# Performance work log

Measured on AMD Instinct MI355X. Metric: run time of the kernel, lower is better.

Reference implementation:

```python
import jax, jax.numpy as jnp
import numpy as np

# fbank band edges (hp.bandmode == 'fbank'), 32 bands over 257 freq bins
EBAND = [0,3,5,8,10,13,15,18,22,25,29,33,38,42,48,53,59,66,73,80,89,97,107,117,128,140,153,167,183,199,216,256]

def _inverse_filter():
    f = np.zeros((len(EBAND), EBAND[-1] + 1), np.float32)
    for i in range(len(EBAND) - 1):
        w = EBAND[i + 1] - EBAND[i]
        for j in range(w):
            f[i, EBAND[i] + j] = 1.0 - j / w
            f[i + 1, EBAND[i] + j] = j / w
    return jnp.asarray(f)  # [32, 257]

def _glin(x, w):
    # GroupedLinear (DeepFilterNet-style, no bias): w [g, in/g, out/g]
    g, gi, go = w.shape
    y = jnp.einsum('...gi,gio->...go', x.reshape(x.shape[:-1] + (g, gi)), w)
    return y.reshape(x.shape[:-1] + (g * go,))

def _prelu(x, a):
    return jnp.where(x >= 0, x, a * x)

def _gru(x, wih, whh, bih, bhh):
    # single-layer torch-style GRU; x [T,B,I], wih/whh [3H, I/H]
    H = whh.shape[-1]
    h0 = jnp.zeros((x.shape[1], H), x.dtype)
    def step(h, xt):
        gi = xt @ wih.T + bih
        gh = h @ whh.T + bhh
        ir, iz, inn = jnp.split(gi, 3, axis=-1)
        hr, hz, hn = jnp.split(gh, 3, axis=-1)
        r = jax.nn.sigmoid(ir + hr)
        z = jax.nn.sigmoid(iz + hz)
        n = jnp.tanh(inn + r * hn)
        hnew = (1.0 - z) * n + z * h
        return hnew, hnew
    _, ys = jax.lax.scan(step, h0, x)
    return ys  # [T,B,H]

def _ggru_layer(x, wih, whh, bih, bhh):
    # grouped GRU layer: weights stacked on leading group axis
    g = wih.shape[0]
    T, B, I = x.shape
    xg = x.reshape(T, B, g, I // g).transpose(2, 0, 1, 3)  # [g,T,B,I/g]
    ys = jax.vmap(_gru)(xg, wih, whh, bih, bhh)            # [g,T,B,H/g]
    return ys.transpose(1, 2, 0, 3).reshape(T, B, -1)

def _shuffle(x, g):
    # channel shuffle between grouped GRU layers
    T, B, H = x.shape
    return x.reshape(T, B, -1, g).swapaxes(2, 3).reshape(T, B, H)

def _forward(main_input, spec, log_power_input, s1_fc_in_w, s1_fc_in_b,
             s1_gru_wih0, s1_gru_whh0, s1_gru_bih0, s1_gru_bhh0,
             s1_gru_wih1, s1_gru_whh1, s1_gru_bih1, s1_gru_bhh1,
             s1_fcout_w, fc_in_low_w, prelu_low, fc_in_high_w, prelu_high,
             gru_low_wih, gru_low_whh, gru_low_bih, gru_low_bhh,
             gru_high_wih, gru_high_whh, gru_high_bih, gru_high_bhh,
             fc_out_low_w, fc_out_high_w, ne, fc):
    B, _, T, F = main_input.shape
    # --- Stage1: pad time, unfold window, keep first ne+1 taps ---
    xp = jnp.pad(main_input, ((0, 0), (0, 0), (ne, ne), (0, 0)))
    win = jnp.stack([xp[:, :, k:k + T] for k in range(ne + 1)], axis=-1)  # [B,1,T,F,ne+1]
    x = win.reshape(B, T, F * (ne + 1))                                   # [B,T,64]
    x0 = (x @ s1_fc_in_w.T + s1_fc_in_b).transpose(1, 0, 2)               # [T,B,32]
    y1 = _gru(x0, s1_gru_wih0, s1_gru_whh0, s1_gru_bih0, s1_gru_bhh0)
    y2 = _gru(y1, s1_gru_wih1, s1_gru_whh1, s1_gru_bih1, s1_gru_bhh1)
    x1 = (y1 + y2).transpose(1, 0, 2)                                     # add_outputs; [B,T,32]
    band_mask = jax.nn.sigmoid(_glin(x1, s1_fcout_w))                     # [B,T,32]
    full_mask = (band_mask @ _inverse_filter()).transpose(0, 2, 1)        # [B,257,T]
    out = spec * full_mask[..., None]                                     # [B,257,T,2]
    # --- low band path ---
    low = jnp.concatenate([log_power_input[:, :, :fc], band_mask], axis=-1)  # [B,T,160]
    low = _prelu(_glin(low, fc_in_low_w), prelu_low).transpose(1, 0, 2)      # [T,B,64]
    acc = jnp.zeros_like(low)
    inp = low
    for l in range(2):  # 2 grouped layers, shuffle between, add_outputs
        inp = _ggru_layer(inp, gru_low_wih[l], gru_low_whh[l], gru_low_bih[l], gru_low_bhh[l])
        if l == 0:
            inp = _shuffle(inp, 2)
        acc = acc + inp
    mask_low = jax.nn.sigmoid(_glin(acc.transpose(1, 0, 2), fc_out_low_w))   # [B,T,128]
    # --- high band path ---
    high = jnp.concatenate([log_power_input[:, :, fc:256], band_mask], axis=-1)  # [B,T,160]
    high = _prelu(_glin(high, fc_in_high_w), prelu_high).transpose(1, 0, 2)      # [T,B,32]
    dfh = _ggru_layer(high, gru_high_wih, gru_high_whh, gru_high_bih, gru_high_bhh)
    mask_high = jax.nn.sigmoid(_glin(dfh.transpose(1, 0, 2), fc_out_high_w))     # [B,T,128]
    # --- fuse masks (rows: 0:fc low, fc:256 high, 256 passthrough) ---
    mask = jnp.concatenate([
        mask_low.transpose(0, 2, 1) * full_mask[:, :fc],
        mask_high.transpose(0, 2, 1) * full_mask[:, fc:256],
        full_mask[:, 256:257],
    ], axis=1)                                                            # [B,257,T]
    spec_out = mask[..., None] * out
    spec_mag = jnp.sqrt(spec_out[..., 0] ** 2 + spec_out[..., 1] ** 2)
    return full_mask, mask, spec_mag, spec_out

def setup_inputs():
    ks = iter(jax.random.split(jax.random.key(0), 48))
    rn = lambda shape, s=1.0: jax.random.normal(next(ks), shape, jnp.float32) * s
    B, T = 256, 256
    return {
        'main_input': rn((B, 1, T, 32)),
        'spec': rn((B, 257, T, 2)),
        'log_power_input': rn((B, T, 256)),
        'n_expand_fbank': 1,
        'freq_cut': 128,
        's1_fc_in_w': rn((32, 64), 0.125),
        's1_fc_in_b': rn((32,), 0.05),
        's1_gru_wih0': rn((96, 32), 0.18),
        's1_gru_whh0': rn((96, 32), 0.18),
        's1_gru_bih0': rn((96,), 0.05),
        's1_gru_bhh0': rn((96,), 0.05),
        's1_gru_wih1': rn((96, 32), 0.18),
        's1_gru_whh1': rn((96, 32), 0.18),
        's1_gru_bih1': rn((96,), 0.05),
        's1_gru_bhh1': rn((96,), 0.05),
        's1_fcout_w': rn((1, 32, 32), 0.18),
        'fc_in_low_w': rn((1, 160, 64), 0.08),
        'prelu_low': jnp.full((1,), 0.25, jnp.float32),
        'fc_in_high_w': rn((2, 80, 16), 0.11),
        'prelu_high': jnp.full((1,), 0.25, jnp.float32),
        'gru_low_wih': rn((2, 2, 96, 32), 0.18),
        'gru_low_whh': rn((2, 2, 96, 32), 0.18),
        'gru_low_bih': rn((2, 2, 96), 0.05),
        'gru_low_bhh': rn((2, 2, 96), 0.05),
        'gru_high_wih': rn((2, 48, 16), 0.25),
        'gru_high_whh': rn((2, 48, 16), 0.25),
        'gru_high_bih': rn((2, 48), 0.05),
        'gru_high_bhh': rn((2, 48), 0.05),
        'fc_out_low_w': rn((1, 64, 128), 0.125),
        'fc_out_high_w': rn((2, 16, 64), 0.25),
    }

def reference(main_input, spec, log_power_input, n_expand_fbank, freq_cut,
              s1_fc_in_w, s1_fc_in_b,
              s1_gru_wih0, s1_gru_whh0, s1_gru_bih0, s1_gru_bhh0,
              s1_gru_wih1, s1_gru_whh1, s1_gru_bih1, s1_gru_bhh1,
              s1_fcout_w, fc_in_low_w, prelu_low, fc_in_high_w, prelu_high,
              gru_low_wih, gru_low_whh, gru_low_bih, gru_low_bhh,
              gru_high_wih, gru_high_whh, gru_high_bih, gru_high_bhh,
              fc_out_low_w, fc_out_high_w):
    return _forward(main_input, spec, log_power_input, s1_fc_in_w, s1_fc_in_b,
                    s1_gru_wih0, s1_gru_whh0, s1_gru_bih0, s1_gru_bhh0,
                    s1_gru_wih1, s1_gru_whh1, s1_gru_bih1, s1_gru_bhh1,
                    s1_fcout_w, fc_in_low_w, prelu_low, fc_in_high_w, prelu_high,
                    gru_low_wih, gru_low_whh, gru_low_bih, gru_low_bhh,
                    gru_high_wih, gru_high_whh, gru_high_bih, gru_high_bhh,
                    fc_out_low_w, fc_out_high_w, int(n_expand_fbank), int(freq_cut))
```

## Files before the change

kernel.cpp:

```cpp
#include <hip/hip_runtime.h>
#include <math.h>

#define Bn 256
#define Tn 256

__constant__ int EB[32] = {0,3,5,8,10,13,15,18,22,25,29,33,38,42,48,53,59,66,73,80,89,97,107,117,128,140,153,167,183,199,216,256};

__device__ __forceinline__ float fsig(float x){ return __builtin_amdgcn_rcpf(1.f + __expf(-x)); }
__device__ __forceinline__ float ftanh(float x){ return 1.f - 2.f*__builtin_amdgcn_rcpf(1.f + __expf(2.f*x)); }

__device__ __forceinline__ void gload16(const float* g, float* l){
  __builtin_amdgcn_global_load_lds((const __attribute__((address_space(1))) void*)g,
                                   (__attribute__((address_space(3))) void*)l, 16, 0, 0);
}

#define KEEP(x) asm volatile("" : "+v"(x))

#define DOT16(res, X, W) do{ float _s0=0.f,_s1=0.f,_s2=0.f,_s3=0.f; \
  _Pragma("unroll") for (int _e=0;_e<4;++_e){ \
    _s0=fmaf((X)[_e],(W)[_e],_s0); _s1=fmaf((X)[4+_e],(W)[4+_e],_s1); \
    _s2=fmaf((X)[8+_e],(W)[8+_e],_s2); _s3=fmaf((X)[12+_e],(W)[12+_e],_s3);} \
  (res)=(_s0+_s1)+(_s2+_s3); }while(0)

#define DOT8(res, X, W) do{ float _s0=0.f,_s1=0.f; \
  _Pragma("unroll") for (int _e=0;_e<4;++_e){ \
    _s0=fmaf((X)[_e],(W)[_e],_s0); _s1=fmaf((X)[4+_e],(W)[4+_e],_s1);} \
  (res)=_s0+_s1; }while(0)

#define FMA44(A, X, W) do{ \
  (A)[0]=fmaf((X).x,(W)[0].x,(A)[0]); (A)[1]=fmaf((X).x,(W)[0].y,(A)[1]); (A)[2]=fmaf((X).x,(W)[0].z,(A)[2]); (A)[3]=fmaf((X).x,(W)[0].w,(A)[3]); \
  (A)[0]=fmaf((X).y,(W)[1].x,(A)[0]); (A)[1]=fmaf((X).y,(W)[1].y,(A)[1]); (A)[2]=fmaf((X).y,(W)[1].z,(A)[2]); (A)[3]=fmaf((X).y,(W)[1].w,(A)[3]); \
  (A)[0]=fmaf((X).z,(W)[2].x,(A)[0]); (A)[1]=fmaf((X).z,(W)[2].y,(A)[1]); (A)[2]=fmaf((X).z,(W)[2].z,(A)[2]); (A)[3]=fmaf((X).z,(W)[2].w,(A)[3]); \
  (A)[0]=fmaf((X).w,(W)[3].x,(A)[0]); (A)[1]=fmaf((X).w,(W)[3].y,(A)[1]); (A)[2]=fmaf((X).w,(W)[3].z,(A)[2]); (A)[3]=fmaf((X).w,(W)[3].w,(A)[3]); \
}while(0)

#define FMA4V(P, AV, S) do{ (P).x=fmaf((AV).x,(S),(P).x); (P).y=fmaf((AV).y,(S),(P).y); \
  (P).z=fmaf((AV).z,(S),(P).z); (P).w=fmaf((AV).w,(S),(P).w); }while(0)

__global__ __launch_bounds__(256) void k0(const float* __restrict__ wfc, const float* __restrict__ bfc,
    const float* __restrict__ wih0, const float* __restrict__ bih0,
    const float* __restrict__ glw_ih, const float* __restrict__ glb_ih,
    const float* __restrict__ ghw_ih, const float* __restrict__ ghb_ih,
    float* __restrict__ wcT, float* __restrict__ bc,
    float* __restrict__ wBT, float* __restrict__ bB){
  int i = blockIdx.x*256 + threadIdx.x;
  if (i < 6144){
    int k = i/96, o = i - (i/96)*96;
    float s = 0.f;
    #pragma unroll
    for (int kk = 0; kk < 32; ++kk) s = fmaf(wih0[o*32+kk], wfc[kk*64+k], s);
    wcT[i] = s;
  } else if (i < 6240){
    int o = i - 6144;
    float s = bih0[o];
    #pragma unroll
    for (int kk = 0; kk < 32; ++kk) s = fmaf(wih0[o*32+kk], bfc[kk], s);
    bc[o] = s;
  } else if (i < 13920){
    int j = i - 6240;
    if (j < 6144){
      int og = j >> 7, rem = j & 127, k = rem >> 2, jj = rem & 3;
      int o = og*4 + jj; int g = o/96, r = o - g*96;
      wBT[j] = glw_ih[(g*96 + r)*32 + k];
    } else {
      int j2 = j - 6144;
      int oh = j2 >> 6, rem = j2 & 63, k = rem >> 2, jj = rem & 3;
      int o = oh*4 + jj; int g = o/48, r = o - g*48;
      wBT[j] = ghw_ih[(g*48 + r)*16 + k];
    }
  } else if (i < 14208){
    int o = i - 13920;
    bB[o] = (o < 192) ? glb_ih[o] : ghb_ih[o - 192];
  }
}

__global__ __launch_bounds__(256) void k1(const float* __restrict__ mi,
    const float* __restrict__ wcT, const float* __restrict__ bc,
    float* __restrict__ gi0){
  __shared__ float mbuf[33*36];
  const int tid = threadIdx.x;
  const int b = blockIdx.x >> 3;
  const int t0 = (blockIdx.x & 7)*32;
  const int bt0 = b*256 + t0;
  for (int idx = tid; idx < 264; idx += 256){
    int row = idx >> 3, c4 = idx & 7;
    int r = t0 - 1 + row;
    float4 v = make_float4(0.f,0.f,0.f,0.f);
    if (r >= 0) v = *(const float4*)&mi[(b*256 + r)*32 + c4*4];
    *(float4*)&mbuf[row*36 + c4*4] = v;
  }
  __syncthreads();
  const int og = tid >> 3, btg = tid & 7;
  if (og >= 24) return;
  float acc[4][4];
  #pragma unroll
  for (int bj = 0; bj < 4; ++bj){ acc[bj][0]=0.f; acc[bj][1]=0.f; acc[bj][2]=0.f; acc[bj][3]=0.f; }
  for (int fq = 0; fq < 8; ++fq){
    float4 wvp[4], wvc[4];
    #pragma unroll
    for (int i = 0; i < 4; ++i){
      int f = fq*4 + i;
      wvp[i] = *(const float4*)&wcT[(2*f)*96 + og*4];
      wvc[i] = *(const float4*)&wcT[(2*f+1)*96 + og*4];
    }
    #pragma unroll
    for (int bj = 0; bj < 4; ++bj){
      int btl = btg + 8*bj;
      float4 xp = *(const float4*)&mbuf[btl*36 + fq*4];
      float4 xc = *(const float4*)&mbuf[(btl+1)*36 + fq*4];
      FMA44(acc[bj], xp, wvp);
      FMA44(acc[bj], xc, wvc);
    }
  }
  float4 bias = *(const float4*)&bc[og*4];
  #pragma unroll
  for (int bj = 0; bj < 4; ++bj){
    int btl = btg + 8*bj;
    float4 o;
    o.x = acc[bj][0] + bias.x; o.y = acc[bj][1] + bias.y;
    o.z = acc[bj][2] + bias.z; o.w = acc[bj][3] + bias.w;
    *(float4*)&gi0[(bt0 + btl)*96 + og*4] = o;
  }
}

__global__ __launch_bounds__(128,1) void kSP(const float* __restrict__ gi0,
    const float* __restrict__ whh0, const float* __restrict__ bhh0,
    const float* __restrict__ wih1, const float* __restrict__ whh1,
    const float* __restrict__ bih1, const float* __restrict__ bhh1,
    const float* __restrict__ fco, float* __restrict__ bmA,
    const float* __restrict__ lpi,
    const float* __restrict__ wlo, const float* __restrict__ whi,
    float* __restrict__ pmid)
{
  __shared__ __attribute__((aligned(16))) float smem[8320];
  const int tid = threadIdx.x;
  if (blockIdx.x < 256){
    float* gib   = smem;
    float* y1buf = smem + 6144;
    float* h1arr = smem + 6208;
    float* h2arr = smem + 6240;
    const int wid = tid >> 6;
    const int lane = tid & 63;
    const int q = lane >> 5, h = lane & 31, ko = q*16;
    const int b = blockIdx.x;
    const float* gsrc = gi0 + b*24576;

    float wI[3][16], wH[3][16], wF[16];
    float b0, b1, b2, b3;
    if (wid == 0){
      #pragma unroll
      for (int g = 0; g < 3; ++g){
        const float* w = whh0 + (g*32+h)*32 + ko;
        #pragma unroll
        for (int k = 0; k < 16; ++k){ wI[g][k] = w[k]; wH[g][k] = w[k]; }
      }
      #pragma unroll
      for (int k = 0; k < 16; ++k) wF[k] = 0.f;
      b0 = bhh0[h]; b1 = bhh0[32+h]; b2 = bhh0[64+h]; b3 = 0.f;
      #pragma unroll
      for (int c0 = 0; c0 < 2; ++c0)
        for (int it = 0; it < 12; ++it)
          gload16(gsrc + c0*3072 + it*256 + lane*4, &gib[c0*3072 + it*256]);
      asm volatile("s_waitcnt vmcnt(0)" ::: "memory");
    } else {
      #pragma unroll
      for (int g = 0; g < 3; ++g){
        const float* wi = wih1 + (g*32+h)*32 + ko;
        const float* wh = whh1 + (g*32+h)*32 + ko;
        #pragma unroll
        for (int k = 0; k < 16; ++k){ wI[g][k] = wi[k]; wH[g][k] = wh[k]; }
      }
      #pragma unroll
      for (int k = 0; k < 16; ++k) wF[k] = fco[(ko+k)*32 + h];
      b0 = bih1[h] + bhh1[h];
      b1 = bih1[32+h] + bhh1[32+h];
      b2 = bih1[64+h];
      b3 = bhh1[64+h];
    }
    #pragma unroll
    for (int g = 0; g < 3; ++g){
      #pragma unroll
      for (int k = 0; k < 16; ++k){ KEEP(wI[g][k]); KEEP(wH[g][k]); }
    }
    #pragma unroll
    for (int k = 0; k < 16; ++k) KEEP(wF[k]);
    __syncthreads();

    float hv[16];
    #pragma unroll
    for (int k = 0; k < 16; ++k) hv[k] = 0.f;
    float hOwn = 0.f;
    float c_r = 0.f, c_z = 0.f, c_n = 0.f, p_r = 0.f, p_z = 0.f, p_n = 0.f;

    for (int s = 0; s <= Tn; ++s){
      __syncthreads();
      if (wid == 0){
        if (s < Tn){
          const int t = s;
          if ((t & 31) == 0){
            if (t){
              int c = t >> 5;
              if (c < 7){
                for (int it = 0; it < 12; ++it)
                  gload16(gsrc + (c+1)*3072 + it*256 + lane*4, &gib[((c+1)&1)*3072 + it*256]);
              }
            }
            const float* gt = &gib[((t>>5)&1)*3072 + (t&31)*96];
            c_r = gt[h]; c_z = gt[32+h]; c_n = gt[64+h];
          } else { c_r = p_r; c_z = p_z; c_n = p_n; }
          if ((t+1) & 31){
            const float* gn = &gib[(((t+1)>>5)&1)*3072 + ((t+1)&31)*96];
            p_r = gn[h]; p_z = gn[32+h]; p_n = gn[64+h];
          }
          float pr, pz, pn;
          DOT16(pr, hv, wI[0]); DOT16(pz, hv, wI[1]); DOT16(pn, hv, wI[2]);
          pr += __shfl_xor(pr,32); pz += __shfl_xor(pz,32); pn += __shfl_xor(pn,32);
          float r = fsig(c_r + pr + b0);
          float z = fsig(c_z + pz + b1);
          float nn = ftanh(c_n + r*(pn + b2));
          float hn = nn + z*(hOwn - nn);
          hOwn = hn;
          h1arr[h] = hn;
          if (q == 0) y1buf[(s & 1)*32 + h] = hn;
          *(float4*)&hv[0]  = *(const float4*)&h1arr[ko+0];
          *(float4*)&hv[4]  = *(const float4*)&h1arr[ko+4];
          *(float4*)&hv[8]  = *(const float4*)&h1arr[ko+8];
          *(float4*)&hv[12] = *(const float4*)&h1arr[ko+12];
        }
      } else {
        if (s >= 1){
          const int t = s - 1;
          const float* yb = &y1buf[(t & 1)*32];
          float xv[16];
          *(float4*)&xv[0]  = *(const float4*)&yb[ko+0];
          *(float4*)&xv[4]  = *(const float4*)&yb[ko+4];
          *(float4*)&xv[8]  = *(const float4*)&yb[ko+8];
          *(float4*)&xv[12] = *(const float4*)&yb[ko+12];
          float ur, uz, ui, vr, vz, vh;
          DOT16(ur, xv, wI[0]); DOT16(uz, xv, wI[1]); DOT16(ui, xv, wI[2]);
          DOT16(vr, hv, wH[0]); DOT16(vz, hv, wH[1]); DOT16(vh, hv, wH[2]);
          float qr = ur + vr, qz = uz + vz;
          qr += __shfl_xor(qr,32); qz += __shfl_xor(qz,32);
          ui += __shfl_xor(ui,32); vh += __shfl_xor(vh,32);
          float r1 = fsig(qr + b0);
          float z1 = fsig(qz + b1);
          float n1 = ftanh(ui + b2 + r1*(vh + b3));
          float hn = n1 + z1*(hOwn - n1);
          hOwn = hn;
          h2arr[h] = hn;
          *(float4*)&hv[0]  = *(const float4*)&h2arr[ko+0];
          *(float4*)&hv[4]  = *(const float4*)&h2arr[ko+4];
          *(float4*)&hv[8]  = *(const float4*)&h2arr[ko+8];
          *(float4*)&hv[12] = *(const float4*)&h2arr[ko+12];
          float sf = 0.f;
          #pragma unroll
          for (int k = 0; k < 16; ++k) sf = fmaf(xv[k] + hv[k], wF[k], sf);
          sf += __shfl_xor(sf,32);
          if (q == 0) bmA[(b*Tn + t)*32 + h] = fsig(sf);
        }
      }
    }
  } else {
    float* xb = smem;
    const int blk = blockIdx.x - 256;
    const int b = blk >> 3;
    const int t0 = (blk & 7)*32;
    const int bt0 = b*256 + t0;
    #pragma unroll
    for (int j = 0; j < 16; ++j){
      int idx = j*128 + tid;
      int row = idx >> 6, c4 = idx & 63;
      float4 v = *(const float4*)&lpi[(bt0 + row)*256 + c4*4];
      *(float4*)&xb[row*260 + c4*4] = v;
    }
    __syncthreads();
    const int og = tid >> 3, btg = tid & 7;
    for (int og2 = og; og2 < 24; og2 += 16){
      float acc[4][4];
      #pragma unroll
      for (int bj = 0; bj < 4; ++bj){ acc[bj][0]=0.f; acc[bj][1]=0.f; acc[bj][2]=0.f; acc[bj][3]=0.f; }
      int obase;
      if (og2 < 16){
        for (int kq = 0; kq < 32; ++kq){
          int k0_ = kq*4;
          float4 wv[4];
          #pragma unroll
          for (int i = 0; i < 4; ++i) wv[i] = *(const float4*)&wlo[(k0_+i)*64 + og2*4];
          #pragma unroll
          for (int bj = 0; bj < 4; ++bj){
            float4 xv = *(const float4*)&xb[(btg + 8*bj)*260 + k0_];
            FMA44(acc[bj], xv, wv);
          }
        }
        obase = og2*4;
      } else {
        int o0 = (og2 - 16)*4;
        int g = o0 >> 4, r0 = o0 & 15;
        int xoff = 128 + g*80;
        int nk = (g == 0) ? 20 : 12;
        for (int kq = 0; kq < nk; ++kq){
          int k0_ = kq*4;
          float4 wv[4];
          #pragma unroll
          for (int i = 0; i < 4; ++i) wv[i] = *(const float4*)&whi[(g*80 + k0_ + i)*16 + r0];
          #pragma unroll
          for (int bj = 0; bj < 4; ++bj){
            float4 xv = *(const float4*)&xb[(btg + 8*bj)*260 + xoff + k0_];
            FMA44(acc[bj], xv, wv);
          }
        }
        obase = 64 + o0;
      }
      #pragma unroll
      for (int bj = 0; bj < 4; ++bj){
        int btl = btg + 8*bj;
        float4 o;
        o.x = acc[bj][0]; o.y = acc[bj][1]; o.z = acc[bj][2]; o.w = acc[bj][3];
        *(float4*)&pmid[(bt0 + btl)*96 + obase] = o;
      }
    }
  }
}

__global__ __launch_bounds__(256) void kPb(const float* __restrict__ bmA,
    const float* __restrict__ pmid,
    const float* __restrict__ wlo, const float* __restrict__ plo,
    const float* __restrict__ whi, const float* __restrict__ phi,
    const float* __restrict__ wBT, const float* __restrict__ bB,
    float* __restrict__ giL, float* __restrict__ giH)
{
  __shared__ float bmb[32*36];
  __shared__ float mb[32*100];
  const int tid = threadIdx.x;
  const int b = blockIdx.x >> 3;
  const int t0 = (blockIdx.x & 7)*32;
  const int bt0 = b*256 + t0;
  {
    int row = tid >> 3, c4 = tid & 7;
    float4 v = *(const float4*)&bmA[(bt0 + row)*32 + c4*4];
    *(float4*)&bmb[row*36 + c4*4] = v;
  }
  __syncthreads();
  const int og = tid >> 3, btg = tid & 7;
  if (og < 16){
    float acc[4][4];
    #pragma unroll
    for (int bj = 0; bj < 4; ++bj){
      float4 p = *(const float4*)&pmid[(bt0 + btg + 8*bj)*96 + og*4];
      acc[bj][0] = p.x; acc[bj][1] = p.y; acc[bj][2] = p.z; acc[bj][3] = p.w;
    }
    for (int kq = 0; kq < 8; ++kq){
      int k0_ = kq*4;
      float4 wv[4];
      #pragma unroll
      for (int i = 0; i < 4; ++i) wv[i] = *(const float4*)&wlo[(128 + k0_ + i)*64 + og*4];
      #pragma unroll
      for (int bj = 0; bj < 4; ++bj){
        float4 xv = *(const float4*)&bmb[(btg + 8*bj)*36 + k0_];
        FMA44(acc[bj], xv, wv);
      }
    }
    const float a = plo[0];
    #pragma unroll
    for (int bj = 0; bj < 4; ++bj){
      float4 m;
      m.x = acc[bj][0] >= 0.f ? acc[bj][0] : a*acc[bj][0];
      m.y = acc[bj][1] >= 0.f ? acc[bj][1] : a*acc[bj][1];
      m.z = acc[bj][2] >= 0.f ? acc[bj][2] : a*acc[bj][2];
      m.w = acc[bj][3] >= 0.f ? acc[bj][3] : a*acc[bj][3];
      *(float4*)&mb[(btg + 8*bj)*100 + og*4] = m;
    }
  } else if (og < 24){
    int o0 = (og - 16)*4;
    int g = o0 >> 4, r0 = o0 & 15;
    float acc[4][4];
    #pragma unroll
    for (int bj = 0; bj < 4; ++bj){
      float4 p = *(const float4*)&pmid[(bt0 + btg + 8*bj)*96 + 64 + o0];
      acc[bj][0] = p.x; acc[bj][1] = p.y; acc[bj][2] = p.z; acc[bj][3] = p.w;
    }
    if (g == 1){
      for (int kq = 0; kq < 8; ++kq){
        int k0_ = 48 + kq*4;
        float4 wv[4];
        #pragma unroll
        for (int i = 0; i < 4; ++i) wv[i] = *(const float4*)&whi[(80 + k0_ + i)*16 + r0];
        #pragma unroll
        for (int bj = 0; bj < 4; ++bj){
          float4 xv = *(const float4*)&bmb[(btg + 8*bj)*36 + kq*4];
          FMA44(acc[bj], xv, wv);
        }
      }
    }
    const float a = phi[0];
    #pragma unroll
    for (int bj = 0; bj < 4; ++bj){
      float4 m;
      m.x = acc[bj][0] >= 0.f ? acc[bj][0] : a*acc[bj][0];
      m.y = acc[bj][1] >= 0.f ? acc[bj][1] : a*acc[bj][1];
      m.z = acc[bj][2] >= 0.f ? acc[bj][2] : a*acc[bj][2];
      m.w = acc[bj][3] >= 0.f ? acc[bj][3] : a*acc[bj][3];
      *(float4*)&mb[(btg + 8*bj)*100 + 64 + o0] = m;
    }
  }
  __syncthreads();
  for (int og2 = og; og2 < 72; og2 += 32){
    int woff, kbase, K, obase, dstride;
    float* dst;
    float4 bias;
    if (og2 < 48){
      woff = og2*128; kbase = (og2 >= 24) ? 32 : 0; K = 32;
      obase = og2*4; dst = giL; dstride = 192;
      bias = *(const float4*)&bB[obase];
    } else {
      int oh = og2 - 48;
      woff = 6144 + oh*64;
      int o0 = oh*4; int g = o0/48;
      kbase = 64 + g*16; K = 16;
      obase = o0; dst = giH; dstride = 96;
      bias = *(const float4*)&bB[192 + o0];
    }
    float acc[4][4];
    #pragma unroll
    for (int bj = 0; bj < 4; ++bj){ acc[bj][0]=0.f; acc[bj][1]=0.f; acc[bj][2]=0.f; acc[bj][3]=0.f; }
    for (int kq = 0; kq < K/4; ++kq){
      float4 wv[4];
      #pragma unroll
      for (int i = 0; i < 4; ++i) wv[i] = *(const float4*)&wBT[woff + (kq*4 + i)*4];
      #pragma unroll
      for (int bj = 0; bj < 4; ++bj){
        float4 xv = *(const float4*)&mb[(btg + 8*bj)*100 + kbase + kq*4];
        FMA44(acc[bj], xv, wv);
      }
    }
    #pragma unroll
    for (int bj = 0; bj < 4; ++bj){
      int btl = btg + 8*bj;
      float4 o;
      o.x = acc[bj][0] + bias.x; o.y = acc[bj][1] + bias.y;
      o.z = acc[bj][2] + bias.z; o.w = acc[bj][3] + bias.w;
      *(float4*)&dst[(bt0 + btl)*dstride + obase] = o;
    }
  }
}

__global__ __launch_bounds__(256,1) void kR2(const float* __restrict__ giL,
    const float* __restrict__ giH,
    const float* __restrict__ wihL, const float* __restrict__ whhL,
    const float* __restrict__ bihL, const float* __restrict__ bhhL,
    const float* __restrict__ whhH, const float* __restrict__ bhhH,
    float* __restrict__ acc, float* __restrict__ dfh)
{
  __shared__ __attribute__((aligned(16))) float smem[12544];
  const int tid = threadIdx.x;
  const int wid = tid >> 6;
  const int lane = tid & 63;
  if (blockIdx.x < 256){
    const int role = wid >> 1;
    const int g = wid & 1;
    const int q = lane >> 5, h = lane & 31, ko = q*16;
    const int b = blockIdx.x;
    float* gib   = smem + g*6144;
    float* y0buf = smem + 12288;
    float* h0arr = smem + 12416 + g*32;
    float* h1l   = smem + 12480;
    const float* gsrc = giL + b*49152 + g*96;

    float wI[3][16], wH[3][16];
    float b0, b1, b2, b3;
    if (role == 0){
      #pragma unroll
      for (int gt = 0; gt < 3; ++gt){
        const float* w = whhL + (g*96 + gt*32 + h)*32 + ko;
        #pragma unroll
        for (int k = 0; k < 16; ++k){ wI[gt][k] = w[k]; wH[gt][k] = w[k]; }
      }
      b0 = bhhL[g*96+h]; b1 = bhhL[g*96+32+h]; b2 = bhhL[g*96+64+h]; b3 = 0.f;
      #pragma unroll
      for (int c0 = 0; c0 < 2; ++c0)
        for (int it = 0; it < 12; ++it){
          int i = it*64 + lane;
          int toff = i/24, c4 = i - toff*24;
          gload16(gsrc + (c0*32 + toff)*192 + c4*4, &gib[c0*3072 + it*256]);
        }
      asm volatile("s_waitcnt vmcnt(0)" ::: "memory");
    } else {
      #pragma unroll
      for (int gt = 0; gt < 3; ++gt){
        const float* wi = wihL + ((2+g)*96 + gt*32 + h)*32 + ko;
        const float* wh = whhL + ((2+g)*96 + gt*32 + h)*32 + ko;
        #pragma unroll
        for (int k = 0; k < 16; ++k){ wI[gt][k] = wi[k]; wH[gt][k] = wh[k]; }
      }
      b0 = bihL[(2+g)*96+h]    + bhhL[(2+g)*96+h];
      b1 = bihL[(2+g)*96+32+h] + bhhL[(2+g)*96+32+h];
      b2 = bihL[(2+g)*96+64+h];
      b3 = bhhL[(2+g)*96+64+h];
    }
    #pragma unroll
    for (int gt = 0; gt < 3; ++gt){
      #pragma unroll
      for (int k = 0; k < 16; ++k){ KEEP(wI[gt][k]); KEEP(wH[gt][k]); }
    }
    __syncthreads();

    float hv[16];
    #pragma unroll
    for (int k = 0; k < 16; ++k) hv[k] = 0.f;
    float hOwn = 0.f;
    float c_r = 0.f, c_z = 0.f, c_n = 0.f, p_r = 0.f, p_z = 0.f, p_n = 0.f;
    const int spos = ((h&1)<<5) + (g<<4) + (h>>1);

    for (int s = 0; s <= Tn; ++s){
      __syncthreads();
      if (role == 0){
        if (s < Tn){
          const int t = s;
          if ((t & 31) == 0){
            if (t){
              int c = t >> 5;
              if (c < 7){
                for (int it = 0; it < 12; ++it){
                  int i = it*64 + lane;
                  int toff = i/24, c4 = i - toff*24;
                  gload16(gsrc + ((c+1)*32 + toff)*192 + c4*4, &gib[((c+1)&1)*3072 + it*256]);
                }
              }
            }
            const float* gt = &gib[((t>>5)&1)*3072 + (t&31)*96];
            c_r = gt[h]; c_z = gt[32+h]; c_n = gt[64+h];
          } else { c_r = p_r; c_z = p_z; c_n = p_n; }
          if ((t+1) & 31){
            const float* gn = &gib[(((t+1)>>5)&1)*3072 + ((t+1)&31)*96];
            p_r = gn[h]; p_z = gn[32+h]; p_n = gn[64+h];
          }
          float pr, pz, pn;
          DOT16(pr, hv, wI[0]); DOT16(pz, hv, wI[1]); DOT16(pn, hv, wI[2]);
          pr += __shfl_xor(pr,32); pz += __shfl_xor(pz,32); pn += __shfl_xor(pn,32);
          float r = fsig(c_r + pr + b0);
          float z = fsig(c_z + pz + b1);
          float nn = ftanh(c_n + r*(pn + b2));
          float hn = nn + z*(hOwn - nn);
          hOwn = hn;
          h0arr[h] = hn;
          if (q == 0) y0buf[(s&1)*64 + spos] = hn;
          *(float4*)&hv[0]  = *(const float4*)&h0arr[ko+0];
          *(float4*)&hv[4]  = *(const float4*)&h0arr[ko+4];
          *(float4*)&hv[8]  = *(const float4*)&h0arr[ko+8];
          *(float4*)&hv[12] = *(const float4*)&h0arr[ko+12];
        }
      } else {
        if (s >= 1){
          const int t = s - 1;
          const float* yb = &y0buf[(t&1)*64];
          float xv[16];
          *(float4*)&xv[0]  = *(const float4*)&yb[g*32 + ko + 0];
          *(float4*)&xv[4]  = *(const float4*)&yb[g*32 + ko + 4];
          *(float4*)&xv[8]  = *(const float4*)&yb[g*32 + ko + 8];
          *(float4*)&xv[12] = *(const float4*)&yb[g*32 + ko + 12];
          float yown = yb[g*32 + h];
          float ur, uz, ui, vr, vz, vh;
          DOT16(ur, xv, wI[0]); DOT16(uz, xv, wI[1]); DOT16(ui, xv, wI[2]);
          DOT16(vr, hv, wH[0]); DOT16(vz, hv, wH[1]); DOT16(vh, hv, wH[2]);
          float qr = ur + vr, qz = uz + vz;
          qr += __shfl_xor(qr,32); qz += __shfl_xor(qz,32);
          ui += __shfl_xor(ui,32); vh += __shfl_xor(vh,32);
          float r1 = fsig(qr + b0);
          float z1 = fsig(qz + b1);
          float n1 = ftanh(ui + b2 + r1*(vh + b3));
          float hn = n1 + z1*(hOwn - n1);
          hOwn = hn;
          h1l[g*32 + h] = hn;
          *(float4*)&hv[0]  = *(const float4*)&h1l[g*32 + ko+0];
          *(float4*)&hv[4]  = *(const float4*)&h1l[g*32 + ko+4];
          *(float4*)&hv[8]  = *(const float4*)&h1l[g*32 + ko+8];
          *(float4*)&hv[12] = *(const float4*)&h1l[g*32 + ko+12];
          if (q == 0) acc[(b*256 + t)*64 + g*32 + h] = yown + hn;
        }
      }
    }
  } else {
    const int g = lane >> 5, qh = (lane >> 4) & 1, h = lane & 15, ko = qh*8;
    const int b = (blockIdx.x - 256)*4 + wid;
    float* gib  = smem + wid*3072;
    float* harr = smem + 12288 + wid*32;
    float ah[3][8];
    #pragma unroll
    for (int gt = 0; gt < 3; ++gt){
      const float* wp = whhH + (g*48 + gt*16 + h)*16 + ko;
      #pragma unroll
      for (int k = 0; k < 8; ++k) ah[gt][k] = wp[k];
    }
    #pragma unroll
    for (int gt = 0; gt < 3; ++gt){
      #pragma unroll
      for (int k = 0; k < 8; ++k) KEEP(ah[gt][k]);
    }
    const float bhr = bhhH[g*48+h], bhz = bhhH[g*48+16+h], bhn = bhhH[g*48+32+h];
    const float* gsrc = giH + b*24576;
    #pragma unroll
    for (int c0 = 0; c0 < 2; ++c0)
      for (int it = 0; it < 6; ++it)
        gload16(gsrc + c0*1536 + it*256 + lane*4, &gib[c0*1536 + it*256]);
    asm volatile("s_waitcnt vmcnt(0)" ::: "memory");

    float hv[8];
    #pragma unroll
    for (int k = 0; k < 8; ++k) hv[k] = 0.f;
    float hOwn = 0.f;
    float c_r = 0.f, c_z = 0.f, c_n = 0.f, p_r = 0.f, p_z = 0.f, p_n = 0.f;

    for (int t = 0; t < Tn; ++t){
      if ((t & 15) == 0){
        if (t){
          int c = t >> 4;
          if (c < 15){
            const float* gs = gsrc + (c+1)*1536;
            for (int it = 0; it < 6; ++it)
              gload16(gs + it*256 + lane*4, &gib[((c+1)&1)*1536 + it*256]);
            asm volatile("s_waitcnt vmcnt(6)" ::: "memory");
          } else {
            asm volatile("s_waitcnt vmcnt(0)" ::: "memory");
          }
        }
        const float* gt = &gib[((t>>4)&1)*1536 + (t&15)*96 + g*48];
        c_r = gt[h]; c_z = gt[16+h]; c_n = gt[32+h];
      } else { c_r = p_r; c_z = p_z; c_n = p_n; }
      if ((t+1) & 15){
        const float* gn = &gib[(((t+1)>>4)&1)*1536 + ((t+1)&15)*96 + g*48];
        p_r = gn[h]; p_z = gn[16+h]; p_n = gn[32+h];
      }
      float pr, pz, pn;
      DOT8(pr, hv, ah[0]); DOT8(pz, hv, ah[1]); DOT8(pn, hv, ah[2]);
      pr += __shfl_xor(pr,16); pz += __shfl_xor(pz,16); pn += __shfl_xor(pn,16);
      float r = fsig(c_r + pr + bhr);
      float z = fsig(c_z + pz + bhz);
      float nn = ftanh(c_n + r*(pn + bhn));
      float hn = nn + z*(hOwn - nn);
      hOwn = hn;
      harr[g*16 + h] = hn;
      *(float4*)&hv[0] = *(const float4*)&harr[g*16 + ko + 0];
      *(float4*)&hv[4] = *(const float4*)&harr[g*16 + ko + 4];
      if (qh == 0) dfh[(b*256 + t)*32 + g*16 + h] = hn;
    }
  }
}

__global__ __launch_bounds__(256) void k7(const float* __restrict__ acc,
    const float* __restrict__ dfh, const float* __restrict__ bmA,
    const float* __restrict__ wlo, const float* __restrict__ whi,
    const float* __restrict__ spec, float* __restrict__ out)
{
  __shared__ float accsT[64*36];
  __shared__ float dfhsT[32*36];
  __shared__ float bmtT[32*36];
  __shared__ float frcs[257];
  __shared__ int   ibds[257];
  const int tid = threadIdx.x;
  const int b  = blockIdx.x >> 3;
  const int t0 = (blockIdx.x & 7) * 32;
  for (int idx = tid; idx < 512; idx += 256){
    int tl = idx >> 4, c4 = (idx & 15)*4;
    float4 v = *(const float4*)&acc[(b*256 + t0 + tl)*64 + c4];
    accsT[(c4+0)*36 + tl] = v.x; accsT[(c4+1)*36 + tl] = v.y;
    accsT[(c4+2)*36 + tl] = v.z; accsT[(c4+3)*36 + tl] = v.w;
  }
  {
    int tl = tid >> 3, c4 = (tid & 7)*4;
    float4 v = *(const float4*)&dfh[(b*256 + t0 + tl)*32 + c4];
    dfhsT[(c4+0)*36 + tl] = v.x; dfhsT[(c4+1)*36 + tl] = v.y;
    dfhsT[(c4+2)*36 + tl] = v.z; dfhsT[(c4+3)*36 + tl] = v.w;
    float4 u = *(const float4*)&bmA[(b*Tn + t0 + tl)*32 + c4];
    bmtT[(c4+0)*36 + tl] = u.x; bmtT[(c4+1)*36 + tl] = u.y;
    bmtT[(c4+2)*36 + tl] = u.z; bmtT[(c4+3)*36 + tl] = u.w;
  }
  for (int f = tid; f < 257; f += 256){
    int i = 0;
    #pragma unroll
    for (int k = 1; k < 31; ++k) if (f >= EB[k]) i = k;
    ibds[f] = i;
    frcs[f] = (f < 256) ? (float)(f - EB[i]) / (float)(EB[i+1] - EB[i]) : 0.f;
  }
  __syncthreads();
  const int fq = tid >> 3, tq = tid & 7;
  float* out1 = out + 16842752;
  float* out2 = out + 2*16842752;
  float* out3 = out + 3*16842752;

  {
    float4 p[4];
    #pragma unroll
    for (int jf = 0; jf < 4; ++jf) p[jf] = make_float4(0.f,0.f,0.f,0.f);
    for (int i = 0; i < 64; ++i){
      float4 av = *(const float4*)&accsT[i*36 + tq*4];
      float4 wv = *(const float4*)&wlo[i*128 + fq*4];
      FMA4V(p[0], av, wv.x); FMA4V(p[1], av, wv.y);
      FMA4V(p[2], av, wv.z); FMA4V(p[3], av, wv.w);
    }
    #pragma unroll
    for (int jf = 0; jf < 4; ++jf){
      int f = fq*4 + jf;
      int i = ibds[f]; float fr = frcs[f];
      float4 b0v = *(const float4*)&bmtT[i*36 + tq*4];
      float4 b1v = *(const float4*)&bmtT[(i+1)*36 + tq*4];
      float4 full;
      full.x = b0v.x*(1.f-fr) + b1v.x*fr; full.y = b0v.y*(1.f-fr) + b1v.y*fr;
      full.z = b0v.z*(1.f-fr) + b1v.z*fr; full.w = b0v.w*(1.f-fr) + b1v.w*fr;
      float4 m;
      m.x = fsig(p[jf].x)*full.x; m.y = fsig(p[jf].y)*full.y;
      m.z = fsig(p[jf].z)*full.z; m.w = fsig(p[jf].w)*full.w;
      int base = (b*257 + f)*Tn + t0 + tq*4;
      float4 s01 = *(const float4*)&spec[base*2];
      float4 s23 = *(const float4*)&spec[base*2 + 4];
      float fm0 = full.x*m.x, fm1 = full.y*m.y, fm2 = full.z*m.z, fm3 = full.w*m.w;
      float sx0 = s01.x*fm0, sy0 = s01.y*fm0;
      float sx1 = s01.z*fm1, sy1 = s01.w*fm1;
      float sx2 = s23.x*fm2, sy2 = s23.y*fm2;
      float sx3 = s23.z*fm3, sy3 = s23.w*fm3;
      *(float4*)&out[base]  = full;
      *(float4*)&out1[base] = m;
      float4 mag;
      mag.x = sqrtf(sx0*sx0 + sy0*sy0); mag.y = sqrtf(sx1*sx1 + sy1*sy1);
      mag.z = sqrtf(sx2*sx2 + sy2*sy2); mag.w = sqrtf(sx3*sx3 + sy3*sy3);
      *(float4*)&out2[base] = mag;
      *(float4*)&out3[base*2]     = make_float4(sx0, sy0, sx1, sy1);
      *(float4*)&out3[base*2 + 4] = make_float4(sx2, sy2, sx3, sy3);
    }
  }
  {
    const int g = fq >> 4;
    const int col = (fq & 15)*4;
    float4 p[4];
    #pragma unroll
    for (int jf = 0; jf < 4; ++jf) p[jf] = make_float4(0.f,0.f,0.f,0.f);
    for (int i = 0; i < 16; ++i){
      float4 dv = *(const float4*)&dfhsT[(g*16 + i)*36 + tq*4];
      float4 wv = *(const float4*)&whi[(g*16 + i)*64 + col];
      FMA4V(p[0], dv, wv.x); FMA4V(p[1], dv, wv.y);
      FMA4V(p[2], dv, wv.z); FMA4V(p[3], dv, wv.w);
    }
    #pragma unroll
    for (int jf = 0; jf < 4; ++jf){
      int f = 128 + fq*4 + jf;
      int i = ibds[f]; float fr = frcs[f];
      float4 b0v = *(const float4*)&bmtT[i*36 + tq*4];
      float4 b1v = *(const float4*)&bmtT[(i+1)*36 + tq*4];
      float4 full;
      full.x = b0v.x*(1.f-fr) + b1v.x*fr; full.y = b0v.y*(1.f-fr) + b1v.y*fr;
      full.z = b0v.z*(1.f-fr) + b1v.z*fr; full.w = b0v.w*(1.f-fr) + b1v.w*fr;
      float4 m;
      m.x = fsig(p[jf].x)*full.x; m.y = fsig(p[jf].y)*full.y;
      m.z = fsig(p[jf].z)*full.z; m.w = fsig(p[jf].w)*full.w;
      int base = (b*257 + f)*Tn + t0 + tq*4;
      float4 s01 = *(const float4*)&spec[base*2];
      float4 s23 = *(const float4*)&spec[base*2 + 4];
      float fm0 = full.x*m.x, fm1 = full.y*m.y, fm2 = full.z*m.z, fm3 = full.w*m.w;
      float sx0 = s01.x*fm0, sy0 = s01.y*fm0;
      float sx1 = s01.z*fm1, sy1 = s01.w*fm1;
      float sx2 = s23.x*fm2, sy2 = s23.y*fm2;
      float sx3 = s23.z*fm3, sy3 = s23.w*fm3;
      *(float4*)&out[base]  = full;
      *(float4*)&out1[base] = m;
      float4 mag;
      mag.x = sqrtf(sx0*sx0 + sy0*sy0); mag.y = sqrtf(sx1*sx1 + sy1*sy1);
      mag.z = sqrtf(sx2*sx2 + sy2*sy2); mag.w = sqrtf(sx3*sx3 + sy3*sy3);
      *(float4*)&out2[base] = mag;
      *(float4*)&out3[base*2]     = make_float4(sx0, sy0, sx1, sy1);
      *(float4*)&out3[base*2 + 4] = make_float4(sx2, sy2, sx3, sy3);
    }
  }
  if (tid < 8){
    int base = (b*257 + 256)*Tn + t0 + tid*4;
    float4 z = make_float4(0.f,0.f,0.f,0.f);
    *(float4*)&out[base]  = z;
    *(float4*)&out1[base] = z;
    *(float4*)&out2[base] = z;
    *(float4*)&out3[base*2]     = z;
    *(float4*)&out3[base*2 + 4] = z;
  }
}

extern "C" void kernel_launch(void* const* d_in, const int* in_sizes, int n_in,
                              void* d_out, int out_size, void* d_ws, size_t ws_size,
                              hipStream_t stream){
  const float* mi   = (const float*)d_in[0];
  const float* spec = (const float*)d_in[1];
  const float* lpi  = (const float*)d_in[2];
  const float* s1w  = (const float*)d_in[5];
  const float* s1b  = (const float*)d_in[6];
  const float* wih0 = (const float*)d_in[7];
  const float* whh0 = (const float*)d_in[8];
  const float* bih0 = (const float*)d_in[9];
  const float* bhh0 = (const float*)d_in[10];
  const float* wih1 = (const float*)d_in[11];
  const float* whh1 = (const float*)d_in[12];
  const float* bih1 = (const float*)d_in[13];
  const float* bhh1 = (const float*)d_in[14];
  const float* fco  = (const float*)d_in[15];
  const float* filw = (const float*)d_in[16];
  const float* plo  = (const float*)d_in[17];
  const float* fihw = (const float*)d_in[18];
  const float* phi  = (const float*)d_in[19];
  const float* glw_ih = (const float*)d_in[20];
  const float* glw_hh = (const float*)d_in[21];
  const float* glb_ih = (const float*)d_in[22];
  const float* glb_hh = (const float*)d_in[23];
  const float* ghw_ih = (const float*)d_in[24];
  const float* ghw_hh = (const float*)d_in[25];
  const float* ghb_ih = (const float*)d_in[26];
  const float* ghb_hh = (const float*)d_in[27];
  const float* folw = (const float*)d_in[28];
  const float* fohw = (const float*)d_in[29];

  float* outf = (float*)d_out;
  float* giL  = outf;
  float* gi0  = outf + 12582912;
  float* giH  = outf + 18874368;

  float* ws   = (float*)d_ws;
  float* wcT  = ws;
  float* bc   = ws + 6144;
  float* wBT  = ws + 6240;
  float* bB   = ws + 13920;
  float* bmA  = ws + 14336;
  float* acc  = ws + 2111488;
  float* dfh  = ws + 6305792;
  float* pmid = ws + 8402944;
  float* out  = (float*)d_out;

  k0<<<56, 256, 0, stream>>>(s1w, s1b, wih0, bih0, glw_ih, glb_ih, ghw_ih, ghb_ih,
                             wcT, bc, wBT, bB);
  k1<<<2048, 256, 0, stream>>>(mi, wcT, bc, gi0);
  kSP<<<2304, 128, 0, stream>>>(gi0, whh0, bhh0, wih1, whh1, bih1, bhh1, fco, bmA,
                                lpi, filw, fihw, pmid);
  kPb<<<2048, 256, 0, stream>>>(bmA, pmid, filw, plo, fihw, phi, wBT, bB, giL, giH);
  kR2<<<320, 256, 0, stream>>>(giL, giH, glw_ih, glw_hh, glb_ih, glb_hh,
                               ghw_hh, ghb_hh, acc, dfh);
  k7<<<2048, 256, 0, stream>>>(acc, dfh, bmA, folw, fohw, spec, out);
}
```

Measured before the change: 483.3 us.

## Process two GRU timesteps per barrier and broadcast hidden state via shuffles

The wavefront-pipelined GRU loops in kSP and kR2 now advance two timesteps per __syncthreads, halving the number of block barriers, with the y buffers widened to hold two steps per parity. The hidden-state broadcast through LDS (write then float4 reads) is replaced by 16 (or 8) __shfl calls per step, removing the LDS round trip. The prefetch of the next timestep's gate inputs is dropped in favour of direct reads. Each shuffle is a ds_bpermute-style cross-lane op, so the broadcast cost may be similar to or higher than the LDS path.

```diff
diff --git a/kernel.cpp b/kernel.cpp
--- a/kernel.cpp
+++ b/kernel.cpp
@@ -137,8 +137,6 @@
   if (blockIdx.x < 256){
     float* gib   = smem;
     float* y1buf = smem + 6144;
-    float* h1arr = smem + 6208;
-    float* h2arr = smem + 6240;
     const int wid = tid >> 6;
     const int lane = tid & 63;
     const int q = lane >> 5, h = lane & 31, ko = q*16;
@@ -190,73 +188,66 @@
     #pragma unroll
     for (int k = 0; k < 16; ++k) hv[k] = 0.f;
     float hOwn = 0.f;
-    float c_r = 0.f, c_z = 0.f, c_n = 0.f, p_r = 0.f, p_z = 0.f, p_n = 0.f;
-
-    for (int s = 0; s <= Tn; ++s){
+
+    for (int e = 0; e <= 128; ++e){
       __syncthreads();
       if (wid == 0){
-        if (s < Tn){
-          const int t = s;
-          if ((t & 31) == 0){
-            if (t){
-              int c = t >> 5;
-              if (c < 7){
-                for (int it = 0; it < 12; ++it)
-                  gload16(gsrc + (c+1)*3072 + it*256 + lane*4, &gib[((c+1)&1)*3072 + it*256]);
-              }
+        if (e < 128){
+          if ((e & 15) == 0 && e){
+            int c = e >> 4;
+            if (c < 7){
+              for (int it = 0; it < 12; ++it)
+                gload16(gsrc + (c+1)*3072 + it*256 + lane*4, &gib[((c+1)&1)*3072 + it*256]);
             }
+          }
+          #pragma unroll
+          for (int j = 0; j < 2; ++j){
+            const int t = 2*e + j;
             const float* gt = &gib[((t>>5)&1)*3072 + (t&31)*96];
-            c_r = gt[h]; c_z = gt[32+h]; c_n = gt[64+h];
-          } else { c_r = p_r; c_z = p_z; c_n = p_n; }
-          if ((t+1) & 31){
-            const float* gn = &gib[(((t+1)>>5)&1)*3072 + ((t+1)&31)*96];
-            p_r = gn[h]; p_z = gn[32+h]; p_n = gn[64+h];
+            float c_r = gt[h], c_z = gt[32+h], c_n = gt[64+h];
+            float pr, pz, pn;
+            DOT16(pr, hv, wI[0]); DOT16(pz, hv, wI[1]); DOT16(pn, hv, wI[2]);
+            pr += __shfl_xor(pr,32); pz += __shfl_xor(pz,32); pn += __shfl_xor(pn,32);
+            float r = fsig(c_r + pr + b0);
+            float z = fsig(c_z + pz + b1);
+            float nn = ftanh(c_n + r*(pn + b2));
+            float hn = nn + z*(hOwn - nn);
+            hOwn = hn;
+            if (q == 0) y1buf[(e & 1)*64 + j*32 + h] = hn;
+            #pragma unroll
+            for (int k = 0; k < 16; ++k) hv[k] = __shfl(hn, ko + k);
           }
-          float pr, pz, pn;
-          DOT16(pr, hv, wI[0]); DOT16(pz, hv, wI[1]); DOT16(pn, hv, wI[2]);
-          pr += __shfl_xor(pr,32); pz += __shfl_xor(pz,32); pn += __shfl_xor(pn,32);
-          float r = fsig(c_r + pr + b0);
-          float z = fsig(c_z + pz + b1);
-          float nn = ftanh(c_n + r*(pn + b2));
-          float hn = nn + z*(hOwn - nn);
-          hOwn = hn;
-          h1arr[h] = hn;
-          if (q == 0) y1buf[(s & 1)*32 + h] = hn;
-          *(float4*)&hv[0]  = *(const float4*)&h1arr[ko+0];
-          *(float4*)&hv[4]  = *(const float4*)&h1arr[ko+4];
-          *(float4*)&hv[8]  = *(const float4*)&h1arr[ko+8];
-          *(float4*)&hv[12] = *(const float4*)&h1arr[ko+12];
         }
       } else {
-        if (s >= 1){
-          const int t = s - 1;
-          const float* yb = &y1buf[(t & 1)*32];
-          float xv[16];
-          *(float4*)&xv[0]  = *(const float4*)&yb[ko+0];
-          *(float4*)&xv[4]  = *(const float4*)&yb[ko+4];
-          *(float4*)&xv[8]  = *(const float4*)&yb[ko+8];
-          *(float4*)&xv[12] = *(const float4*)&yb[ko+12];
-          float ur, uz, ui, vr, vz, vh;
-          DOT16(ur, xv, wI[0]); DOT16(uz, xv, wI[1]); DOT16(ui, xv, wI[2]);
-          DOT16(vr, hv, wH[0]); DOT16(vz, hv, wH[1]); DOT16(vh, hv, wH[2]);
-          float qr = ur + vr, qz = uz + vz;
-          qr += __shfl_xor(qr,32); qz += __shfl_xor(qz,32);
-          ui += __shfl_xor(ui,32); vh += __shfl_xor(vh,32);
-          float r1 = fsig(qr + b0);
-          float z1 = fsig(qz + b1);
-          float n1 = ftanh(ui + b2 + r1*(vh + b3));
-          float hn = n1 + z1*(hOwn - n1);
-          hOwn = hn;
-          h2arr[h] = hn;
-          *(float4*)&hv[0]  = *(const float4*)&h2arr[ko+0];
-          *(float4*)&hv[4]  = *(const float4*)&h2arr[ko+4];
-          *(float4*)&hv[8]  = *(const float4*)&h2arr[ko+8];
-          *(float4*)&hv[12] = *(const float4*)&h2arr[ko+12];
-          float sf = 0.f;
+        if (e >= 1){
           #pragma unroll
-          for (int k = 0; k < 16; ++k) sf = fmaf(xv[k] + hv[k], wF[k], sf);
-          sf += __shfl_xor(sf,32);
-          if (q == 0) bmA[(b*Tn + t)*32 + h] = fsig(sf);
+          for (int j = 0; j < 2; ++j){
+            const int t = 2*(e-1) + j;
+            const float* yb = &y1buf[((e-1) & 1)*64 + j*32];
+            float xv[16];
+            *(float4*)&xv[0]  = *(const float4*)&yb[ko+0];
+            *(float4*)&xv[4]  = *(const float4*)&yb[ko+4];
+            *(float4*)&xv[8]  = *(const float4*)&yb[ko+8];
+            *(float4*)&xv[12] = *(const float4*)&yb[ko+12];
+            float ur, uz, ui, vr, vz, vh;
+            DOT16(ur, xv, wI[0]); DOT16(uz, xv, wI[1]); DOT16(ui, xv, wI[2]);
+            DOT16(vr, hv, wH[0]); DOT16(vz, hv, wH[1]); DOT16(vh, hv, wH[2]);
+            float qr = ur + vr, qz = uz + vz;
+            qr += __shfl_xor(qr,32); qz += __shfl_xor(qz,32);
+            ui += __shfl_xor(ui,32); vh += __shfl_xor(vh,32);
+            float r1 = fsig(qr + b0);
+            float z1 = fsig(qz + b1);
+            float n1 = ftanh(ui + b2 + r1*(vh + b3));
+            float hn = n1 + z1*(hOwn - n1);
+            hOwn = hn;
+            #pragma unroll
+            for (int k = 0; k < 16; ++k) hv[k] = __shfl(hn, ko + k);
+            float sf = 0.f;
+            #pragma unroll
+            for (int k = 0; k < 16; ++k) sf = fmaf(xv[k] + hv[k], wF[k], sf);
+            sf += __shfl_xor(sf,32);
+            if (q == 0) bmA[(b*Tn + t)*32 + h] = fsig(sf);
+          }
         }
       }
     }
@@ -462,8 +453,6 @@
     const int b = blockIdx.x;
     float* gib   = smem + g*6144;
     float* y0buf = smem + 12288;
-    float* h0arr = smem + 12416 + g*32;
-    float* h1l   = smem + 12480;
     const float* gsrc = giL + b*49152 + g*96;
 
     float wI[3][16], wH[3][16];
@@ -508,74 +497,67 @@
     #pragma unroll
     for (int k = 0; k < 16; ++k) hv[k] = 0.f;
     float hOwn = 0.f;
-    float c_r = 0.f, c_z = 0.f, c_n = 0.f, p_r = 0.f, p_z = 0.f, p_n = 0.f;
     const int spos = ((h&1)<<5) + (g<<4) + (h>>1);
 
-    for (int s = 0; s <= Tn; ++s){
+    for (int e = 0; e <= 128; ++e){
       __syncthreads();
       if (role == 0){
-        if (s < Tn){
-          const int t = s;
-          if ((t & 31) == 0){
-            if (t){
-              int c = t >> 5;
-              if (c < 7){
-                for (int it = 0; it < 12; ++it){
-                  int i = it*64 + lane;
-                  int toff = i/24, c4 = i - toff*24;
-                  gload16(gsrc + ((c+1)*32 + toff)*192 + c4*4, &gib[((c+1)&1)*3072 + it*256]);
-                }
+        if (e < 128){
+          if ((e & 15) == 0 && e){
+            int c = e >> 4;
+            if (c < 7){
+              for (int it = 0; it < 12; ++it){
+                int i = it*64 + lane;
+                int toff = i/24, c4 = i - toff*24;
+                gload16(gsrc + ((c+1)*32 + toff)*192 + c4*4, &gib[((c+1)&1)*3072 + it*256]);
               }
             }
+          }
+          #pragma unroll
+          for (int j = 0; j < 2; ++j){
+            const int t = 2*e + j;
             const float* gt = &gib[((t>>5)&1)*3072 + (t&31)*96];
-            c_r = gt[h]; c_z = gt[32+h]; c_n = gt[64+h];
-          } else { c_r = p_r; c_z = p_z; c_n = p_n; }
-          if ((t+1) & 31){
-            const float* gn = &gib[(((t+1)>>5)&1)*3072 + ((t+1)&31)*96];
-            p_r = gn[h]; p_z = gn[32+h]; p_n = gn[64+h];
+            float c_r = gt[h], c_z = gt[32+h], c_n = gt[64+h];
+            float pr, pz, pn;
+            DOT16(pr, hv, wI[0]); DOT16(pz, hv, wI[1]); DOT16(pn, hv, wI[2]);
+            pr += __shfl_xor(pr,32); pz += __shfl_xor(pz,32); pn += __shfl_xor(pn,32);
+            float r = fsig(c_r + pr + b0);
+            float z = fsig(c_z + pz + b1);
+            float nn = ftanh(c_n + r*(pn + b2));
+            float hn = nn + z*(hOwn - nn);
+            hOwn = hn;
+            if (q == 0) y0buf[(e&1)*128 + j*64 + spos] = hn;
+            #pragma unroll
+            for (int k = 0; k < 16; ++k) hv[k] = __shfl(hn, ko + k);
           }
-          float pr, pz, pn;
-          DOT16(pr, hv, wI[0]); DOT16(pz, hv, wI[1]); DOT16(pn, hv, wI[2]);
-          pr += __shfl_xor(pr,32); pz += __shfl_xor(pz,32); pn += __shfl_xor(pn,32);
-          float r = fsig(c_r + pr + b0);
-          float z = fsig(c_z + pz + b1);
-          float nn = ftanh(c_n + r*(pn + b2));
-          float hn = nn + z*(hOwn - nn);
-          hOwn = hn;
-          h0arr[h] = hn;
-          if (q == 0) y0buf[(s&1)*64 + spos] = hn;
-          *(float4*)&hv[0]  = *(const float4*)&h0arr[ko+0];
-          *(float4*)&hv[4]  = *(const float4*)&h0arr[ko+4];
-          *(float4*)&hv[8]  = *(const float4*)&h0arr[ko+8];
-          *(float4*)&hv[12] = *(const float4*)&h0arr[ko+12];
         }
       } else {
-        if (s >= 1){
-          const int t = s - 1;
-          const float* yb = &y0buf[(t&1)*64];
-          float xv[16];
-          *(float4*)&xv[0]  = *(const float4*)&yb[g*32 + ko + 0];
-          *(float4*)&xv[4]  = *(const float4*)&yb[g*32 + ko + 4];
-          *(float4*)&xv[8]  = *(const float4*)&yb[g*32 + ko + 8];
-          *(float4*)&xv[12] = *(const float4*)&yb[g*32 + ko + 12];
-          float yown = yb[g*32 + h];
-          float ur, uz, ui, vr, vz, vh;
-          DOT16(ur, xv, wI[0]); DOT16(uz, xv, wI[1]); DOT16(ui, xv, wI[2]);
-          DOT16(vr, hv, wH[0]); DOT16(vz, hv, wH[1]); DOT16(vh, hv, wH[2]);
-          float qr = ur + vr, qz = uz + vz;
-          qr += __shfl_xor(qr,32); qz += __shfl_xor(qz,32);
-          ui += __shfl_xor(ui,32); vh += __shfl_xor(vh,32);
-          float r1 = fsig(qr + b0);
-          float z1 = fsig(qz + b1);
-          float n1 = ftanh(ui + b2 + r1*(vh + b3));
-          float hn = n1 + z1*(hOwn - n1);
-          hOwn = hn;
-          h1l[g*32 + h] = hn;
-          *(float4*)&hv[0]  = *(const float4*)&h1l[g*32 + ko+0];
-          *(float4*)&hv[4]  = *(const float4*)&h1l[g*32 + ko+4];
-          *(float4*)&hv[8]  = *(const float4*)&h1l[g*32 + ko+8];
-          *(float4*)&hv[12] = *(const float4*)&h1l[g*32 + ko+12];
-          if (q == 0) acc[(b*256 + t)*64 + g*32 + h] = yown + hn;
+        if (e >= 1){
+          #pragma unroll
+          for (int j = 0; j < 2; ++j){
+            const int t = 2*(e-1) + j;
+            const float* yb = &y0buf[((e-1)&1)*128 + j*64];
+            float xv[16];
+            *(float4*)&xv[0]  = *(const float4*)&yb[g*32 + ko + 0];
+            *(float4*)&xv[4]  = *(const float4*)&yb[g*32 + ko + 4];
+            *(float4*)&xv[8]  = *(const float4*)&yb[g*32 + ko + 8];
+            *(float4*)&xv[12] = *(const float4*)&yb[g*32 + ko + 12];
+            float yown = yb[g*32 + h];
+            float ur, uz, ui, vr, vz, vh;
+            DOT16(ur, xv, wI[0]); DOT16(uz, xv, wI[1]); DOT16(ui, xv, wI[2]);
+            DOT16(vr, hv, wH[0]); DOT16(vz, hv, wH[1]); DOT16(vh, hv, wH[2]);
+            float qr = ur + vr, qz = uz + vz;
+            qr += __shfl_xor(qr,32); qz += __shfl_xor(qz,32);
+            ui += __shfl_xor(ui,32); vh += __shfl_xor(vh,32);
+            float r1 = fsig(qr + b0);
+            float z1 = fsig(qz + b1);
+            float n1 = ftanh(ui + b2 + r1*(vh + b3));
+            float hn = n1 + z1*(hOwn - n1);
+            hOwn = hn;
+            #pragma unroll
+            for (int k = 0; k < 16; ++k) hv[k] = __shfl(hn, ko + k);
+            if (q == 0) acc[(b*256 + t)*64 + g*32 + h] = yown + hn;
+          }
         }
       }
     }
@@ -583,7 +565,6 @@
     const int g = lane >> 5, qh = (lane >> 4) & 1, h = lane & 15, ko = qh*8;
     const int b = (blockIdx.x - 256)*4 + wid;
     float* gib  = smem + wid*3072;
-    float* harr = smem + 12288 + wid*32;
     float ah[3][8];
     #pragma unroll
     for (int gt = 0; gt < 3; ++gt){
@@ -638,9 +619,8 @@
       float nn = ftanh(c_n + r*(pn + bhn));
       float hn = nn + z*(hOwn - nn);
       hOwn = hn;
-      harr[g*16 + h] = hn;
-      *(float4*)&hv[0] = *(const float4*)&harr[g*16 + ko + 0];
-      *(float4*)&hv[4] = *(const float4*)&harr[g*16 + ko + 4];
+      #pragma unroll
+      for (int k = 0; k < 8; ++k) hv[k] = __shfl(hn, g*32 + ko + k);
       if (qh == 0) dfh[(b*256 + t)*32 + g*16 + h] = hn;
     }
   }
```

After: 509.1 us. 5.3% more time.
